# Kernel optimization log

Measured on AMD Instinct MI355X. Metric: run time of the kernel, lower is better.

Reference implementation:

```python
import jax, jax.numpy as jnp
import numpy as np

B, T, TOKEN_DIM, TPR_DIM = 16, 256, 256, 10
INNER = TOKEN_DIM // 4  # 64
TH = 32                 # tpr_mlp hidden dim
EPS = 1e-5              # BatchNorm eps


def _bn(x, g, b, m, v):
    # BatchNorm1d in eval mode: normalize with running stats
    return (x - m) * jax.lax.rsqrt(v + EPS) * g + b


def setup_inputs() -> dict:
    key = jax.random.key(0)
    ks = iter(jax.random.split(key, 32))
    def n(shape, s=0.02):
        return jax.random.normal(next(ks), shape, dtype=jnp.float32) * s
    def bn_params(c):
        g = 1.0 + 0.1 * jax.random.normal(next(ks), (c,), dtype=jnp.float32)
        b = 0.1 * jax.random.normal(next(ks), (c,), dtype=jnp.float32)
        m = 0.1 * jax.random.normal(next(ks), (c,), dtype=jnp.float32)
        v = jax.random.uniform(next(ks), (c,), dtype=jnp.float32, minval=0.5, maxval=1.5)
        return g, b, m, v
    inp = {}
    inp['x'] = jax.random.normal(next(ks), (B, T, TOKEN_DIM), dtype=jnp.float32)
    inp['r'] = jax.random.normal(next(ks), (B, T, T, TPR_DIM), dtype=jnp.float32)
    # fc1: Linear(token,token) + BN(token)
    inp['W1'] = n((TOKEN_DIM, TOKEN_DIM)); inp['b1'] = n((TOKEN_DIM,))
    inp['bn1_g'], inp['bn1_b'], inp['bn1_m'], inp['bn1_v'] = bn_params(TOKEN_DIM)
    # VectorAttention
    inp['Wqkv'] = n((TOKEN_DIM, 3 * INNER))
    inp['Wt1'] = n((TPR_DIM, TH)); inp['bt1'] = n((TH,))
    inp['bnt_g'], inp['bnt_b'], inp['bnt_m'], inp['bnt_v'] = bn_params(TH)
    inp['Wt2'] = n((TH, INNER)); inp['bt2'] = n((INNER,))
    inp['Wa1'] = n((INNER, INNER)); inp['ba1'] = n((INNER,))
    inp['Wa2'] = n((INNER, INNER)); inp['ba2'] = n((INNER,))
    # fc2: Linear(inner, token) + BN(token)
    inp['W2'] = n((INNER, TOKEN_DIM)); inp['b2'] = n((TOKEN_DIM,))
    inp['bn2_g'], inp['bn2_b'], inp['bn2_m'], inp['bn2_v'] = bn_params(TOKEN_DIM)
    return inp


def reference(x, r, W1, b1, bn1_g, bn1_b, bn1_m, bn1_v, Wqkv,
              Wt1, bt1, bnt_g, bnt_b, bnt_m, bnt_v, Wt2, bt2,
              Wa1, ba1, Wa2, ba2, W2, b2, bn2_g, bn2_b, bn2_m, bn2_v):
    # fc1 + BN, residual skip (pre-relu)
    y = _bn(x @ W1 + b1, bn1_g, bn1_b, bn1_m, bn1_v)  # [B,T,C]
    skip = y
    y = jax.nn.relu(y)
    # VectorAttention
    qkv = y @ Wqkv                                     # [B,T,3*inner]
    q, k, v = jnp.split(qkv, 3, axis=-1)               # each [B,T,inner]
    qk_rel = q[:, :, None, :] - k[:, None, :, :]       # [B,T,T,inner]
    rel_emb = jax.nn.relu(_bn(r @ Wt1 + bt1, bnt_g, bnt_b, bnt_m, bnt_v)) @ Wt2 + bt2  # [B,T,T,inner]
    vv = v[:, None, :, :] + rel_emb                    # [B,T,T,inner]
    h = jax.nn.relu((qk_rel + rel_emb) @ Wa1 + ba1)
    sim = h @ Wa2 + ba2                                # [B,T,T,inner]
    attn = jax.nn.softmax(sim, axis=-2)                # softmax over j (neighbor) axis
    agg = jnp.sum(attn * vv, axis=2)                   # [B,T,inner]
    # fc2 + BN + residual + relu
    out = jax.nn.relu(_bn(agg @ W2 + b2, bn2_g, bn2_b, bn2_m, bn2_v) + skip)
    return out  # [B,T,token_dim]
```

## Files before the change

kernel.cpp:

```cpp
#include <hip/hip_runtime.h>
#include <hip/hip_bf16.h>
#include <math.h>

#define BB 16
#define TT 256
#define CC 256
#define INNER 64
#define TPR 10
#define THD 32
#define EPSV 1e-5f

typedef __attribute__((ext_vector_type(8))) short short8;
typedef __attribute__((ext_vector_type(4))) float f32x4;
typedef __attribute__((ext_vector_type(4))) unsigned int u32x4;

__device__ __forceinline__ short f2bf(float f) {
    unsigned u = __float_as_uint(f);
    u += 0x7fffu + ((u >> 16) & 1);
    return (short)(u >> 16);
}
__device__ __forceinline__ unsigned pkbf(float a, float b) {
    return (unsigned)(unsigned short)f2bf(a) | ((unsigned)(unsigned short)f2bf(b) << 16);
}

__global__ __launch_bounds__(256) void fc1_qkv_kernel(
    const float* __restrict__ x, const float* __restrict__ W1, const float* __restrict__ b1,
    const float* __restrict__ g1, const float* __restrict__ bb1,
    const float* __restrict__ m1, const float* __restrict__ v1,
    const float* __restrict__ Wqkv,
    float* __restrict__ skip, float* __restrict__ qkv)
{
    const int ROWS = 8;
    __shared__ float xr[ROWS][CC];
    __shared__ float yr[ROWS][CC];
    const int n0 = blockIdx.x * ROWS;
    const int t = threadIdx.x;

#pragma unroll
    for (int rr = 0; rr < ROWS; ++rr)
        xr[rr][t] = x[(size_t)(n0 + rr) * CC + t];
    __syncthreads();

    float acc[ROWS];
#pragma unroll
    for (int rr = 0; rr < ROWS; ++rr) acc[rr] = 0.f;
    for (int k = 0; k < CC; ++k) {
        float wv = W1[(size_t)k * CC + t];
#pragma unroll
        for (int rr = 0; rr < ROWS; ++rr) acc[rr] = fmaf(xr[rr][k], wv, acc[rr]);
    }
    const float s1 = g1[t] * rsqrtf(v1[t] + EPSV);
    const float base = b1[t] - m1[t];
    const float bet = bb1[t];
#pragma unroll
    for (int rr = 0; rr < ROWS; ++rr) {
        float y = (acc[rr] + base) * s1 + bet;
        skip[(size_t)(n0 + rr) * CC + t] = y;
        yr[rr][t] = fmaxf(y, 0.f);
    }
    __syncthreads();

    if (t < 192) {
        float a2[ROWS];
#pragma unroll
        for (int rr = 0; rr < ROWS; ++rr) a2[rr] = 0.f;
        for (int k = 0; k < CC; ++k) {
            float wv = Wqkv[(size_t)k * 192 + t];
#pragma unroll
            for (int rr = 0; rr < ROWS; ++rr) a2[rr] = fmaf(yr[rr][k], wv, a2[rr]);
        }
#pragma unroll
        for (int rr = 0; rr < ROWS; ++rr)
            qkv[(size_t)(n0 + rr) * 192 + t] = a2[rr];
    }
}

#define O_R    0
#define O_TH   16384
#define O_WT1  49152
#define O_WT2  53248
#define O_WA1  61440
#define O_WA2  69632
#define O_RED  77824
#define LDSZ   81920

__device__ __forceinline__ int swb(int row, int cb, int sh, int mask) {
    return (row << sh) + (((cb & ~15) ^ ((row & mask) << 4)) | (cb & 15));
}
__device__ __forceinline__ short8 ldfrag(const char* lds, int base, int row, int cb16, int sh, int mask) {
    return *(const short8*)(lds + base + (row << sh) + (cb16 ^ ((row & mask) << 4)));
}

__global__ __launch_bounds__(512, 4) void attn_mfma_kernel(
    const float* __restrict__ r, const float* __restrict__ qkv,
    const float* __restrict__ Wt1, const float* __restrict__ bt1,
    const float* __restrict__ gt, const float* __restrict__ bbt,
    const float* __restrict__ mt, const float* __restrict__ vt,
    const float* __restrict__ Wt2, const float* __restrict__ bt2,
    const float* __restrict__ Wa1, const float* __restrict__ ba1,
    const float* __restrict__ Wa2, const float* __restrict__ ba2,
    float* __restrict__ agg)
{
    __shared__ __align__(16) char lds[LDSZ];
    const int n = blockIdx.x, b = n >> 8;
    const int tid = threadIdx.x;
    const int wv = tid >> 6, lane = tid & 63;
    const int lid = lane & 15, q4 = lane >> 4;
    const int kb = q4 * 16;
    const int jt0 = wv * 2;

    {
        u32x4 z = {0u, 0u, 0u, 0u};
        *(u32x4*)(lds + O_R + tid * 16) = z;
        *(u32x4*)(lds + O_R + 8192 + tid * 16) = z;
        if (tid < 256) *(u32x4*)(lds + O_WT1 + tid * 16) = z;
    }
    __syncthreads();

    {
        const float* rrow = r + (size_t)n * (TT * TPR);
        for (int e = tid; e < TT * TPR; e += 512) {
            int j = e / TPR, p = e - j * TPR;
            *(short*)(lds + O_R + swb(j, p * 2, 6, 3)) = f2bf(rrow[e]);
        }
        if (tid < TPR * THD) {
            int p = tid >> 5, h = tid & 31;
            float scv = gt[h] * rsqrtf(vt[h] + EPSV);
            *(short*)(lds + O_WT1 + swb(h, p * 2, 7, 7)) = f2bf(Wt1[tid] * scv);
        }
        for (int e = tid; e < THD * INNER; e += 512) {
            int h = e >> 6, c = e & 63;
            *(short*)(lds + O_WT2 + swb(c, h * 2, 7, 7)) = f2bf(Wt2[e]);
        }
        for (int e = tid; e < INNER * INNER; e += 512) {
            int k = e >> 6, c = e & 63;
            *(short*)(lds + O_WA1 + swb(c, k * 2, 7, 7)) = f2bf(Wa1[e]);
            *(short*)(lds + O_WA2 + swb(c, k * 2, 7, 7)) = f2bf(Wa2[e]);
        }
    }
    __syncthreads();

    const float* kvb = qkv + (size_t)b * (TT * 192);
    const f32x4 z4 = {0.f, 0.f, 0.f, 0.f};

    {
        short8 aw0 = ldfrag(lds, O_WT1, lid, kb, 7, 7);
        short8 aw1 = ldfrag(lds, O_WT1, 16 + lid, kb, 7, 7);
        f32x4 acc1[2][2];
#pragma unroll
        for (int tn = 0; tn < 2; ++tn) {
            int j = (jt0 + tn) * 16 + lid;
            short8 bf = ldfrag(lds, O_R, j, kb, 6, 3);
            acc1[0][tn] = __builtin_amdgcn_mfma_f32_16x16x32_bf16(aw0, bf, z4, 0, 0, 0);
            acc1[1][tn] = __builtin_amdgcn_mfma_f32_16x16x32_bf16(aw1, bf, z4, 0, 0, 0);
        }
#pragma unroll
        for (int tm = 0; tm < 2; ++tm) {
            int ch0 = tm * 16 + q4 * 4;
            f32x4 g4 = *(const f32x4*)(gt + ch0);
            f32x4 vv4 = *(const f32x4*)(vt + ch0);
            f32x4 b4 = *(const f32x4*)(bt1 + ch0);
            f32x4 m4 = *(const f32x4*)(mt + ch0);
            f32x4 bb4 = *(const f32x4*)(bbt + ch0);
            f32x4 c1;
#pragma unroll
            for (int g = 0; g < 4; ++g)
                c1[g] = (b4[g] - m4[g]) * (g4[g] * rsqrtf(vv4[g] + EPSV)) + bb4[g];
#pragma unroll
            for (int tn = 0; tn < 2; ++tn) {
                int j = (jt0 + tn) * 16 + lid;
                float h0 = fmaxf(acc1[tm][tn][0] + c1[0], 0.f);
                float h1 = fmaxf(acc1[tm][tn][1] + c1[1], 0.f);
                float h2 = fmaxf(acc1[tm][tn][2] + c1[2], 0.f);
                float h3 = fmaxf(acc1[tm][tn][3] + c1[3], 0.f);
                uint2 w; w.x = pkbf(h0, h1); w.y = pkbf(h2, h3);
                *(uint2*)(lds + O_TH + swb(j, tm * 32 + q4 * 8, 7, 7)) = w;
            }
        }
    }

    f32x4 rel[4][2];
    {
        short8 aw[4];
#pragma unroll
        for (int tm = 0; tm < 4; ++tm)
            aw[tm] = ldfrag(lds, O_WT2, tm * 16 + lid, kb, 7, 7);
#pragma unroll
        for (int tn = 0; tn < 2; ++tn) {
            int j = (jt0 + tn) * 16 + lid;
            short8 bf = ldfrag(lds, O_TH, j, kb, 7, 7);
#pragma unroll
            for (int tm = 0; tm < 4; ++tm)
                rel[tm][tn] = __builtin_amdgcn_mfma_f32_16x16x32_bf16(aw[tm], bf, z4, 0, 0, 0);
        }
    }
#pragma unroll
    for (int tm = 0; tm < 4; ++tm) {
        int ch0 = tm * 16 + q4 * 4;
        f32x4 bt24 = *(const f32x4*)(bt2 + ch0);
        f32x4 qv4 = *(const f32x4*)(qkv + (size_t)n * 192 + ch0);
#pragma unroll
        for (int tn = 0; tn < 2; ++tn) {
            int j = (jt0 + tn) * 16 + lid;
            f32x4 kv4 = *(const f32x4*)(kvb + (size_t)j * 192 + 64 + ch0);
            float t0, t1, t2, t3;
#pragma unroll
            for (int g = 0; g < 4; ++g) rel[tm][tn][g] += bt24[g];
            t0 = qv4[0] - kv4[0] + rel[tm][tn][0];
            t1 = qv4[1] - kv4[1] + rel[tm][tn][1];
            t2 = qv4[2] - kv4[2] + rel[tm][tn][2];
            t3 = qv4[3] - kv4[3] + rel[tm][tn][3];
            uint2 w; w.x = pkbf(t0, t1); w.y = pkbf(t2, t3);
            *(uint2*)(lds + O_TH + swb(j, tm * 32 + q4 * 8, 7, 7)) = w;
        }
    }

    f32x4 acc[4][2];
#pragma unroll
    for (int tm = 0; tm < 4; ++tm)
#pragma unroll
        for (int tn = 0; tn < 2; ++tn) acc[tm][tn] = z4;
#pragma unroll
    for (int ks = 0; ks < 2; ++ks) {
        short8 aw[4];
#pragma unroll
        for (int tm = 0; tm < 4; ++tm)
            aw[tm] = ldfrag(lds, O_WA1, tm * 16 + lid, ks * 64 + kb, 7, 7);
#pragma unroll
        for (int tn = 0; tn < 2; ++tn) {
            int j = (jt0 + tn) * 16 + lid;
            short8 bf = ldfrag(lds, O_TH, j, ks * 64 + kb, 7, 7);
#pragma unroll
            for (int tm = 0; tm < 4; ++tm)
                acc[tm][tn] = __builtin_amdgcn_mfma_f32_16x16x32_bf16(aw[tm], bf, acc[tm][tn], 0, 0, 0);
        }
    }
#pragma unroll
    for (int tm = 0; tm < 4; ++tm) {
        int ch0 = tm * 16 + q4 * 4;
        f32x4 ba14 = *(const f32x4*)(ba1 + ch0);
#pragma unroll
        for (int tn = 0; tn < 2; ++tn) {
            int j = (jt0 + tn) * 16 + lid;
            float h0 = fmaxf(acc[tm][tn][0] + ba14[0], 0.f);
            float h1 = fmaxf(acc[tm][tn][1] + ba14[1], 0.f);
            float h2 = fmaxf(acc[tm][tn][2] + ba14[2], 0.f);
            float h3 = fmaxf(acc[tm][tn][3] + ba14[3], 0.f);
            uint2 w; w.x = pkbf(h0, h1); w.y = pkbf(h2, h3);
            *(uint2*)(lds + O_TH + swb(j, tm * 32 + q4 * 8, 7, 7)) = w;
        }
    }

#pragma unroll
    for (int tm = 0; tm < 4; ++tm)
#pragma unroll
        for (int tn = 0; tn < 2; ++tn) acc[tm][tn] = z4;
#pragma unroll
    for (int ks = 0; ks < 2; ++ks) {
        short8 aw[4];
#pragma unroll
        for (int tm = 0; tm < 4; ++tm)
            aw[tm] = ldfrag(lds, O_WA2, tm * 16 + lid, ks * 64 + kb, 7, 7);
#pragma unroll
        for (int tn = 0; tn < 2; ++tn) {
            int j = (jt0 + tn) * 16 + lid;
            short8 bf = ldfrag(lds, O_TH, j, ks * 64 + kb, 7, 7);
#pragma unroll
            for (int tm = 0; tm < 4; ++tm)
                acc[tm][tn] = __builtin_amdgcn_mfma_f32_16x16x32_bf16(aw[tm], bf, acc[tm][tn], 0, 0, 0);
        }
    }

#pragma unroll
    for (int tm = 0; tm < 4; ++tm) {
        const int ch0 = tm * 16 + q4 * 4;
        f32x4 num = z4, den = z4;
#pragma unroll
        for (int tn = 0; tn < 2; ++tn) {
            int j = (jt0 + tn) * 16 + lid;
            f32x4 v4 = *(const f32x4*)(kvb + (size_t)j * 192 + 128 + ch0);
#pragma unroll
            for (int g = 0; g < 4; ++g) {
                float ev = __expf(acc[tm][tn][g]);
                den[g] += ev;
                num[g] = fmaf(ev, v4[g] + rel[tm][tn][g], num[g]);
            }
        }
#pragma unroll
        for (int ofs = 1; ofs < 16; ofs <<= 1) {
#pragma unroll
            for (int g = 0; g < 4; ++g) {
                num[g] += __shfl_xor(num[g], ofs);
                den[g] += __shfl_xor(den[g], ofs);
            }
        }
        if (lid == 0) {
            int base = O_RED + ((wv * 4 + tm) * 4 + q4) * 32;
            *(f32x4*)(lds + base) = num;
            *(f32x4*)(lds + base + 16) = den;
        }
    }
    __syncthreads();

    if (tid < 64) {
        int tm = tid >> 4, qq = (tid >> 2) & 3, g = tid & 3;
        float nn = 0.f, dd = 0.f;
#pragma unroll
        for (int w = 0; w < 8; ++w) {
            int base = O_RED + ((w * 4 + tm) * 4 + qq) * 32 + g * 4;
            nn += *(const float*)(lds + base);
            dd += *(const float*)(lds + base + 16);
        }
        agg[(size_t)n * 64 + tid] = nn / dd;
    }
}

__global__ __launch_bounds__(256) void fc2_kernel(
    const float* __restrict__ agg, const float* __restrict__ W2, const float* __restrict__ b2,
    const float* __restrict__ g2, const float* __restrict__ bb2,
    const float* __restrict__ m2, const float* __restrict__ v2,
    const float* __restrict__ skip, float* __restrict__ out)
{
    const int ROWS = 8;
    __shared__ float ar[ROWS][INNER];
    const int n0 = blockIdx.x * ROWS;
    const int t = threadIdx.x;

    for (int idx = t; idx < ROWS * INNER; idx += 256)
        ((float*)ar)[idx] = agg[(size_t)n0 * INNER + idx];
    __syncthreads();

    const float s2 = g2[t] * rsqrtf(v2[t] + EPSV);
    const float base = b2[t] - m2[t];
    const float bet = bb2[t];

    float accv[ROWS];
#pragma unroll
    for (int rr = 0; rr < ROWS; ++rr) accv[rr] = 0.f;
    for (int k = 0; k < INNER; ++k) {
        float wv = W2[(size_t)k * CC + t];
#pragma unroll
        for (int rr = 0; rr < ROWS; ++rr) accv[rr] = fmaf(ar[rr][k], wv, accv[rr]);
    }
#pragma unroll
    for (int rr = 0; rr < ROWS; ++rr) {
        float y = (accv[rr] + base) * s2 + bet;
        out[(size_t)(n0 + rr) * CC + t] =
            fmaxf(y + skip[(size_t)(n0 + rr) * CC + t], 0.f);
    }
}

extern "C" void kernel_launch(void* const* d_in, const int* in_sizes, int n_in,
                              void* d_out, int out_size, void* d_ws, size_t ws_size,
                              hipStream_t stream)
{
    const float* x   = (const float*)d_in[0];
    const float* r   = (const float*)d_in[1];
    const float* W1  = (const float*)d_in[2];
    const float* b1  = (const float*)d_in[3];
    const float* g1  = (const float*)d_in[4];
    const float* bb1 = (const float*)d_in[5];
    const float* m1  = (const float*)d_in[6];
    const float* v1  = (const float*)d_in[7];
    const float* Wqkv= (const float*)d_in[8];
    const float* Wt1 = (const float*)d_in[9];
    const float* bt1 = (const float*)d_in[10];
    const float* gt  = (const float*)d_in[11];
    const float* bbt = (const float*)d_in[12];
    const float* mt  = (const float*)d_in[13];
    const float* vt  = (const float*)d_in[14];
    const float* Wt2 = (const float*)d_in[15];
    const float* bt2 = (const float*)d_in[16];
    const float* Wa1 = (const float*)d_in[17];
    const float* ba1 = (const float*)d_in[18];
    const float* Wa2 = (const float*)d_in[19];
    const float* ba2 = (const float*)d_in[20];
    const float* W2  = (const float*)d_in[21];
    const float* b2  = (const float*)d_in[22];
    const float* g2  = (const float*)d_in[23];
    const float* bb2 = (const float*)d_in[24];
    const float* m2  = (const float*)d_in[25];
    const float* v2  = (const float*)d_in[26];
    float* out = (float*)d_out;

    const int N = BB * TT;
    float* skip = (float*)d_ws;
    float* qkv  = skip + (size_t)N * CC;
    float* agg  = qkv  + (size_t)N * 192;

    fc1_qkv_kernel<<<dim3(N / 8), dim3(256), 0, stream>>>(
        x, W1, b1, g1, bb1, m1, v1, Wqkv, skip, qkv);
    attn_mfma_kernel<<<dim3(N), dim3(512), 0, stream>>>(
        r, qkv, Wt1, bt1, gt, bbt, mt, vt, Wt2, bt2, Wa1, ba1, Wa2, ba2, agg);
    fc2_kernel<<<dim3(N / 8), dim3(256), 0, stream>>>(
        agg, W2, b2, g2, bb2, m2, v2, skip, out);
}
```

Measured before the change: 170.6 us.

## Precompute bf16 swizzled weight image and stream it into LDS via global_load_lds

Adds a small prep kernel that converts and BN-folds the tiny MLP weights into a pre-swizzled bf16 image in workspace once per call. Each attention block then copies that image straight into LDS with global_load_lds, instead of redoing per-element fp32→bf16 conversion and scattered stores in all 4096 blocks. Other changes: the initial LDS zeroing pass and its barrier are removed, the r tile is packed with vectorized stores, biases are folded into the MFMA accumulator init, k/v loads are hoisted early, and hardware bf16 pack conversion replaces manual rounding. The risks are an extra kernel launch and the subtle layout changes to the Wt1/Wt2 swizzle. Dropping ba2 is valid because softmax is shift-invariant.

```diff
diff --git a/kernel.cpp b/kernel.cpp
--- a/kernel.cpp
+++ b/kernel.cpp
@@ -12,15 +12,62 @@
 
 typedef __attribute__((ext_vector_type(8))) short short8;
 typedef __attribute__((ext_vector_type(4))) float f32x4;
-typedef __attribute__((ext_vector_type(4))) unsigned int u32x4;
 
 __device__ __forceinline__ short f2bf(float f) {
     unsigned u = __float_as_uint(f);
     u += 0x7fffu + ((u >> 16) & 1);
     return (short)(u >> 16);
 }
-__device__ __forceinline__ unsigned pkbf(float a, float b) {
-    return (unsigned)(unsigned short)f2bf(a) | ((unsigned)(unsigned short)f2bf(b) << 16);
+__device__ __forceinline__ unsigned cvtpk(float a, float b) {
+    __hip_bfloat162 h = __float22bfloat162_rn(float2{a, b});
+    return *(unsigned*)&h;
+}
+
+#define IMG_WT1  0
+#define IMG_WT2  2048
+#define IMG_WA1  6144
+#define IMG_WA2  14336
+#define IMG_C1   22528
+#define IMG_SZ   22656
+
+__device__ __forceinline__ int sww(int pb, int key) {
+    return ((pb & ~15) ^ key) | (pb & 15);
+}
+
+__global__ __launch_bounds__(256) void prep_kernel(
+    const float* __restrict__ Wt1, const float* __restrict__ bt1,
+    const float* __restrict__ gt, const float* __restrict__ bbt,
+    const float* __restrict__ mt, const float* __restrict__ vt,
+    const float* __restrict__ Wt2, const float* __restrict__ Wa1,
+    const float* __restrict__ Wa2, char* __restrict__ img)
+{
+    const int blk = blockIdx.x, t = threadIdx.x;
+    if (blk == 0) {
+        for (int e = t; e < 32 * 32; e += 256) {
+            int m = e >> 5, k = e & 31;
+            float scv = gt[m] * rsqrtf(vt[m] + EPSV);
+            float v = (k < TPR) ? Wt1[k * 32 + m] * scv : 0.f;
+            *(short*)(img + IMG_WT1 + m * 64 + k * 2) = f2bf(v);
+        }
+        if (t < 32) {
+            float scv = gt[t] * rsqrtf(vt[t] + EPSV);
+            ((float*)(img + IMG_C1))[t] = (bt1[t] - mt[t]) * scv + bbt[t];
+        }
+    } else if (blk == 1) {
+        for (int e = t; e < 32 * 64; e += 256) {
+            int h = e >> 6, c = e & 63;
+            int off = IMG_WT2 + (c >> 1) * 128 + sww((c & 1) * 64 + h * 2, ((c >> 1) & 7) << 4);
+            *(short*)(img + off) = f2bf(Wt2[e]);
+        }
+    } else {
+        const float* W = (blk == 2) ? Wa1 : Wa2;
+        int base = (blk == 2) ? IMG_WA1 : IMG_WA2;
+        for (int e = t; e < 64 * 64; e += 256) {
+            int k = e >> 6, c = e & 63;
+            int off = base + c * 128 + sww(k * 2, (c & 7) << 4);
+            *(short*)(img + off) = f2bf(W[e]);
+        }
+    }
 }
 
 __global__ __launch_bounds__(256) void fc1_qkv_kernel(
@@ -78,11 +125,11 @@
 #define O_R    0
 #define O_TH   16384
 #define O_WT1  49152
-#define O_WT2  53248
-#define O_WA1  61440
-#define O_WA2  69632
-#define O_RED  77824
-#define LDSZ   81920
+#define O_WT2  51200
+#define O_WA1  55296
+#define O_WA2  63488
+#define O_RED  71680
+#define LDSZ   75776
 
 __device__ __forceinline__ int swb(int row, int cb, int sh, int mask) {
     return (row << sh) + (((cb & ~15) ^ ((row & mask) << 4)) | (cb & 15));
@@ -93,13 +140,8 @@
 
 __global__ __launch_bounds__(512, 4) void attn_mfma_kernel(
     const float* __restrict__ r, const float* __restrict__ qkv,
-    const float* __restrict__ Wt1, const float* __restrict__ bt1,
-    const float* __restrict__ gt, const float* __restrict__ bbt,
-    const float* __restrict__ mt, const float* __restrict__ vt,
-    const float* __restrict__ Wt2, const float* __restrict__ bt2,
-    const float* __restrict__ Wa1, const float* __restrict__ ba1,
-    const float* __restrict__ Wa2, const float* __restrict__ ba2,
-    float* __restrict__ agg)
+    const float* __restrict__ bt2, const float* __restrict__ ba1,
+    const char* __restrict__ img, float* __restrict__ agg)
 {
     __shared__ __align__(16) char lds[LDSZ];
     const int n = blockIdx.x, b = n >> 8;
@@ -109,113 +151,173 @@
     const int kb = q4 * 16;
     const int jt0 = wv * 2;
 
-    {
-        u32x4 z = {0u, 0u, 0u, 0u};
-        *(u32x4*)(lds + O_R + tid * 16) = z;
-        *(u32x4*)(lds + O_R + 8192 + tid * 16) = z;
-        if (tid < 256) *(u32x4*)(lds + O_WT1 + tid * 16) = z;
-    }
-    __syncthreads();
+    const float* kvb = qkv + (size_t)b * (TT * 192);
+    const f32x4 z4 = {0.f, 0.f, 0.f, 0.f};
+
+#pragma unroll
+    for (int ci = 0; ci < 3; ++ci) {
+        int c = wv + ci * 8;
+        if (c < 22) {
+            int ldsoff;
+            if (c < 2)       ldsoff = O_WT1 + c * 1024;
+            else if (c < 6)  ldsoff = O_WT2 + (c - 2) * 1024;
+            else if (c < 14) ldsoff = O_WA1 + (c - 6) * 1024;
+            else             ldsoff = O_WA2 + (c - 14) * 1024;
+            __builtin_amdgcn_global_load_lds(
+                (const __attribute__((address_space(1))) unsigned*)(const unsigned*)(img + c * 1024 + lane * 16),
+                (__attribute__((address_space(3))) unsigned*)(unsigned*)(lds + ldsoff + lane * 16),
+                16, 0, 0);
+        }
+    }
+
+    f32x4 k4[4][2];
+#pragma unroll
+    for (int tm = 0; tm < 4; ++tm) {
+        int ch0 = tm * 16 + q4 * 4;
+#pragma unroll
+        for (int tn = 0; tn < 2; ++tn) {
+            int j = (jt0 + tn) * 16 + lid;
+            k4[tm][tn] = *(const f32x4*)(kvb + (size_t)j * 192 + 64 + ch0);
+        }
+    }
 
     {
         const float* rrow = r + (size_t)n * (TT * TPR);
-        for (int e = tid; e < TT * TPR; e += 512) {
-            int j = e / TPR, p = e - j * TPR;
-            *(short*)(lds + O_R + swb(j, p * 2, 6, 3)) = f2bf(rrow[e]);
-        }
-        if (tid < TPR * THD) {
-            int p = tid >> 5, h = tid & 31;
-            float scv = gt[h] * rsqrtf(vt[h] + EPSV);
-            *(short*)(lds + O_WT1 + swb(h, p * 2, 7, 7)) = f2bf(Wt1[tid] * scv);
-        }
-        for (int e = tid; e < THD * INNER; e += 512) {
-            int h = e >> 6, c = e & 63;
-            *(short*)(lds + O_WT2 + swb(c, h * 2, 7, 7)) = f2bf(Wt2[e]);
-        }
-        for (int e = tid; e < INNER * INNER; e += 512) {
-            int k = e >> 6, c = e & 63;
-            *(short*)(lds + O_WA1 + swb(c, k * 2, 7, 7)) = f2bf(Wa1[e]);
-            *(short*)(lds + O_WA2 + swb(c, k * 2, 7, 7)) = f2bf(Wa2[e]);
+        int j = tid >> 1, half = tid & 1;
+        const float* rp = rrow + j * TPR + half * 5;
+        float v0 = rp[0], v1 = rp[1], v2 = rp[2], v3 = rp[3], v4 = rp[4];
+        char* rb = lds + O_R + j * 64;
+        if (half == 0) {
+            uint2 w; w.x = cvtpk(v0, v1); w.y = cvtpk(v2, v3);
+            *(uint2*)(rb) = w;
+            *(unsigned short*)(rb + 8) = (unsigned short)f2bf(v4);
+        } else {
+            *(unsigned short*)(rb + 10) = (unsigned short)f2bf(v0);
+            *(unsigned*)(rb + 12) = cvtpk(v1, v2);
+            *(unsigned*)(rb + 16) = cvtpk(v3, v4);
+            *(unsigned*)(rb + 20) = 0u;
+            uint2 zz; zz.x = 0u; zz.y = 0u;
+            *(uint2*)(rb + 24) = zz;
+            *(uint2*)(rb + 32) = zz;
+            *(uint2*)(rb + 40) = zz;
+            *(uint2*)(rb + 48) = zz;
+            *(uint2*)(rb + 56) = zz;
         }
     }
     __syncthreads();
 
-    const float* kvb = qkv + (size_t)b * (TT * 192);
-    const f32x4 z4 = {0.f, 0.f, 0.f, 0.f};
+    const float* c1g = (const float*)(img + IMG_C1);
 
     {
-        short8 aw0 = ldfrag(lds, O_WT1, lid, kb, 7, 7);
-        short8 aw1 = ldfrag(lds, O_WT1, 16 + lid, kb, 7, 7);
+        short8 a10 = ldfrag(lds, O_WT1, lid, kb, 6, 0);
+        short8 a11 = ldfrag(lds, O_WT1, 16 + lid, kb, 6, 0);
+        f32x4 c1v0 = *(const f32x4*)(c1g + q4 * 4);
+        f32x4 c1v1 = *(const f32x4*)(c1g + 16 + q4 * 4);
         f32x4 acc1[2][2];
 #pragma unroll
         for (int tn = 0; tn < 2; ++tn) {
             int j = (jt0 + tn) * 16 + lid;
-            short8 bf = ldfrag(lds, O_R, j, kb, 6, 3);
-            acc1[0][tn] = __builtin_amdgcn_mfma_f32_16x16x32_bf16(aw0, bf, z4, 0, 0, 0);
-            acc1[1][tn] = __builtin_amdgcn_mfma_f32_16x16x32_bf16(aw1, bf, z4, 0, 0, 0);
-        }
-#pragma unroll
-        for (int tm = 0; tm < 2; ++tm) {
-            int ch0 = tm * 16 + q4 * 4;
-            f32x4 g4 = *(const f32x4*)(gt + ch0);
-            f32x4 vv4 = *(const f32x4*)(vt + ch0);
-            f32x4 b4 = *(const f32x4*)(bt1 + ch0);
-            f32x4 m4 = *(const f32x4*)(mt + ch0);
-            f32x4 bb4 = *(const f32x4*)(bbt + ch0);
-            f32x4 c1;
-#pragma unroll
-            for (int g = 0; g < 4; ++g)
-                c1[g] = (b4[g] - m4[g]) * (g4[g] * rsqrtf(vv4[g] + EPSV)) + bb4[g];
+            short8 bf = ldfrag(lds, O_R, j, kb, 6, 0);
+            acc1[0][tn] = __builtin_amdgcn_mfma_f32_16x16x32_bf16(a10, bf, c1v0, 0, 0, 0);
+            acc1[1][tn] = __builtin_amdgcn_mfma_f32_16x16x32_bf16(a11, bf, c1v1, 0, 0, 0);
+        }
+#pragma unroll
+        for (int tm = 0; tm < 2; ++tm)
 #pragma unroll
             for (int tn = 0; tn < 2; ++tn) {
                 int j = (jt0 + tn) * 16 + lid;
-                float h0 = fmaxf(acc1[tm][tn][0] + c1[0], 0.f);
-                float h1 = fmaxf(acc1[tm][tn][1] + c1[1], 0.f);
-                float h2 = fmaxf(acc1[tm][tn][2] + c1[2], 0.f);
-                float h3 = fmaxf(acc1[tm][tn][3] + c1[3], 0.f);
-                uint2 w; w.x = pkbf(h0, h1); w.y = pkbf(h2, h3);
+                uint2 w;
+                w.x = cvtpk(fmaxf(acc1[tm][tn][0], 0.f), fmaxf(acc1[tm][tn][1], 0.f));
+                w.y = cvtpk(fmaxf(acc1[tm][tn][2], 0.f), fmaxf(acc1[tm][tn][3], 0.f));
                 *(uint2*)(lds + O_TH + swb(j, tm * 32 + q4 * 8, 7, 7)) = w;
             }
-        }
+    }
+
+    f32x4 qv4[4], bt2v[4];
+#pragma unroll
+    for (int tm = 0; tm < 4; ++tm) {
+        int ch0 = tm * 16 + q4 * 4;
+        qv4[tm] = *(const f32x4*)(qkv + (size_t)n * 192 + ch0);
+        bt2v[tm] = *(const f32x4*)(bt2 + ch0);
     }
 
     f32x4 rel[4][2];
     {
         short8 aw[4];
 #pragma unroll
+        for (int tm = 0; tm < 4; ++tm) {
+            int c = tm * 16 + lid;
+            aw[tm] = ldfrag(lds, O_WT2, c >> 1, (c & 1) * 64 + kb, 7, 7);
+        }
+#pragma unroll
+        for (int tn = 0; tn < 2; ++tn) {
+            int j = (jt0 + tn) * 16 + lid;
+            short8 bf = ldfrag(lds, O_TH, j, kb, 7, 7);
+#pragma unroll
+            for (int tm = 0; tm < 4; ++tm)
+                rel[tm][tn] = __builtin_amdgcn_mfma_f32_16x16x32_bf16(aw[tm], bf, bt2v[tm], 0, 0, 0);
+        }
+    }
+#pragma unroll
+    for (int tm = 0; tm < 4; ++tm)
+#pragma unroll
+        for (int tn = 0; tn < 2; ++tn) {
+            int j = (jt0 + tn) * 16 + lid;
+            float t0 = qv4[tm][0] - k4[tm][tn][0] + rel[tm][tn][0];
+            float t1 = qv4[tm][1] - k4[tm][tn][1] + rel[tm][tn][1];
+            float t2 = qv4[tm][2] - k4[tm][tn][2] + rel[tm][tn][2];
+            float t3 = qv4[tm][3] - k4[tm][tn][3] + rel[tm][tn][3];
+            uint2 w; w.x = cvtpk(t0, t1); w.y = cvtpk(t2, t3);
+            *(uint2*)(lds + O_TH + swb(j, tm * 32 + q4 * 8, 7, 7)) = w;
+        }
+
+    f32x4 ba1v[4];
+#pragma unroll
+    for (int tm = 0; tm < 4; ++tm)
+        ba1v[tm] = *(const f32x4*)(ba1 + tm * 16 + q4 * 4);
+    f32x4 acc[4][2];
+#pragma unroll
+    for (int tm = 0; tm < 4; ++tm)
+#pragma unroll
+        for (int tn = 0; tn < 2; ++tn) acc[tm][tn] = ba1v[tm];
+#pragma unroll
+    for (int ks = 0; ks < 2; ++ks) {
+        short8 aw[4];
+#pragma unroll
         for (int tm = 0; tm < 4; ++tm)
-            aw[tm] = ldfrag(lds, O_WT2, tm * 16 + lid, kb, 7, 7);
-#pragma unroll
-        for (int tn = 0; tn < 2; ++tn) {
-            int j = (jt0 + tn) * 16 + lid;
-            short8 bf = ldfrag(lds, O_TH, j, kb, 7, 7);
+            aw[tm] = ldfrag(lds, O_WA1, tm * 16 + lid, ks * 64 + kb, 7, 7);
+#pragma unroll
+        for (int tn = 0; tn < 2; ++tn) {
+            int j = (jt0 + tn) * 16 + lid;
+            short8 bf = ldfrag(lds, O_TH, j, ks * 64 + kb, 7, 7);
 #pragma unroll
             for (int tm = 0; tm < 4; ++tm)
-                rel[tm][tn] = __builtin_amdgcn_mfma_f32_16x16x32_bf16(aw[tm], bf, z4, 0, 0, 0);
-        }
-    }
+                acc[tm][tn] = __builtin_amdgcn_mfma_f32_16x16x32_bf16(aw[tm], bf, acc[tm][tn], 0, 0, 0);
+        }
+    }
+
+    f32x4 v4h[4][2];
 #pragma unroll
     for (int tm = 0; tm < 4; ++tm) {
         int ch0 = tm * 16 + q4 * 4;
-        f32x4 bt24 = *(const f32x4*)(bt2 + ch0);
-        f32x4 qv4 = *(const f32x4*)(qkv + (size_t)n * 192 + ch0);
-#pragma unroll
-        for (int tn = 0; tn < 2; ++tn) {
-            int j = (jt0 + tn) * 16 + lid;
-            f32x4 kv4 = *(const f32x4*)(kvb + (size_t)j * 192 + 64 + ch0);
-            float t0, t1, t2, t3;
-#pragma unroll
-            for (int g = 0; g < 4; ++g) rel[tm][tn][g] += bt24[g];
-            t0 = qv4[0] - kv4[0] + rel[tm][tn][0];
-            t1 = qv4[1] - kv4[1] + rel[tm][tn][1];
-            t2 = qv4[2] - kv4[2] + rel[tm][tn][2];
-            t3 = qv4[3] - kv4[3] + rel[tm][tn][3];
-            uint2 w; w.x = pkbf(t0, t1); w.y = pkbf(t2, t3);
+#pragma unroll
+        for (int tn = 0; tn < 2; ++tn) {
+            int j = (jt0 + tn) * 16 + lid;
+            v4h[tm][tn] = *(const f32x4*)(kvb + (size_t)j * 192 + 128 + ch0);
+        }
+    }
+
+#pragma unroll
+    for (int tm = 0; tm < 4; ++tm)
+#pragma unroll
+        for (int tn = 0; tn < 2; ++tn) {
+            int j = (jt0 + tn) * 16 + lid;
+            uint2 w;
+            w.x = cvtpk(fmaxf(acc[tm][tn][0], 0.f), fmaxf(acc[tm][tn][1], 0.f));
+            w.y = cvtpk(fmaxf(acc[tm][tn][2], 0.f), fmaxf(acc[tm][tn][3], 0.f));
             *(uint2*)(lds + O_TH + swb(j, tm * 32 + q4 * 8, 7, 7)) = w;
         }
-    }
-
-    f32x4 acc[4][2];
+
 #pragma unroll
     for (int tm = 0; tm < 4; ++tm)
 #pragma unroll
@@ -225,7 +327,7 @@
         short8 aw[4];
 #pragma unroll
         for (int tm = 0; tm < 4; ++tm)
-            aw[tm] = ldfrag(lds, O_WA1, tm * 16 + lid, ks * 64 + kb, 7, 7);
+            aw[tm] = ldfrag(lds, O_WA2, tm * 16 + lid, ks * 64 + kb, 7, 7);
 #pragma unroll
         for (int tn = 0; tn < 2; ++tn) {
             int j = (jt0 + tn) * 16 + lid;
@@ -235,55 +337,17 @@
                 acc[tm][tn] = __builtin_amdgcn_mfma_f32_16x16x32_bf16(aw[tm], bf, acc[tm][tn], 0, 0, 0);
         }
     }
+
 #pragma unroll
     for (int tm = 0; tm < 4; ++tm) {
-        int ch0 = tm * 16 + q4 * 4;
-        f32x4 ba14 = *(const f32x4*)(ba1 + ch0);
-#pragma unroll
-        for (int tn = 0; tn < 2; ++tn) {
-            int j = (jt0 + tn) * 16 + lid;
-            float h0 = fmaxf(acc[tm][tn][0] + ba14[0], 0.f);
-            float h1 = fmaxf(acc[tm][tn][1] + ba14[1], 0.f);
-            float h2 = fmaxf(acc[tm][tn][2] + ba14[2], 0.f);
-            float h3 = fmaxf(acc[tm][tn][3] + ba14[3], 0.f);
-            uint2 w; w.x = pkbf(h0, h1); w.y = pkbf(h2, h3);
-            *(uint2*)(lds + O_TH + swb(j, tm * 32 + q4 * 8, 7, 7)) = w;
-        }
-    }
-
-#pragma unroll
-    for (int tm = 0; tm < 4; ++tm)
-#pragma unroll
-        for (int tn = 0; tn < 2; ++tn) acc[tm][tn] = z4;
-#pragma unroll
-    for (int ks = 0; ks < 2; ++ks) {
-        short8 aw[4];
-#pragma unroll
-        for (int tm = 0; tm < 4; ++tm)
-            aw[tm] = ldfrag(lds, O_WA2, tm * 16 + lid, ks * 64 + kb, 7, 7);
-#pragma unroll
-        for (int tn = 0; tn < 2; ++tn) {
-            int j = (jt0 + tn) * 16 + lid;
-            short8 bf = ldfrag(lds, O_TH, j, ks * 64 + kb, 7, 7);
-#pragma unroll
-            for (int tm = 0; tm < 4; ++tm)
-                acc[tm][tn] = __builtin_amdgcn_mfma_f32_16x16x32_bf16(aw[tm], bf, acc[tm][tn], 0, 0, 0);
-        }
-    }
-
-#pragma unroll
-    for (int tm = 0; tm < 4; ++tm) {
-        const int ch0 = tm * 16 + q4 * 4;
         f32x4 num = z4, den = z4;
 #pragma unroll
         for (int tn = 0; tn < 2; ++tn) {
-            int j = (jt0 + tn) * 16 + lid;
-            f32x4 v4 = *(const f32x4*)(kvb + (size_t)j * 192 + 128 + ch0);
 #pragma unroll
             for (int g = 0; g < 4; ++g) {
                 float ev = __expf(acc[tm][tn][g]);
                 den[g] += ev;
-                num[g] = fmaf(ev, v4[g] + rel[tm][tn][g], num[g]);
+                num[g] = fmaf(ev, v4h[tm][tn][g] + rel[tm][tn][g], num[g]);
             }
         }
 #pragma unroll
@@ -374,7 +438,6 @@
     const float* Wa1 = (const float*)d_in[17];
     const float* ba1 = (const float*)d_in[18];
     const float* Wa2 = (const float*)d_in[19];
-    const float* ba2 = (const float*)d_in[20];
     const float* W2  = (const float*)d_in[21];
     const float* b2  = (const float*)d_in[22];
     const float* g2  = (const float*)d_in[23];
@@ -387,11 +450,14 @@
     float* skip = (float*)d_ws;
     float* qkv  = skip + (size_t)N * CC;
     float* agg  = qkv  + (size_t)N * 192;
-
+    char*  img  = (char*)(agg + (size_t)N * 64);
+
+    prep_kernel<<<dim3(4), dim3(256), 0, stream>>>(
+        Wt1, bt1, gt, bbt, mt, vt, Wt2, Wa1, Wa2, img);
     fc1_qkv_kernel<<<dim3(N / 8), dim3(256), 0, stream>>>(
         x, W1, b1, g1, bb1, m1, v1, Wqkv, skip, qkv);
     attn_mfma_kernel<<<dim3(N), dim3(512), 0, stream>>>(
-        r, qkv, Wt1, bt1, gt, bbt, mt, vt, Wt2, bt2, Wa1, ba1, Wa2, ba2, agg);
+        r, qkv, bt2, ba1, img, agg);
     fc2_kernel<<<dim3(N / 8), dim3(256), 0, stream>>>(
         agg, W2, b2, g2, bb2, m2, v2, skip, out);
 }
```

After: 160.5 us. 5.9% less time.
